# Kernel optimization log

Hardware: AMD Instinct MI355X
Metric: run time of the kernel (lower is better)

The kernel has to match this reference:

```python
import jax, jax.numpy as jnp
import numpy as np

K0 = 5.0
ISIZE = (1024.0, 1024.0)  # image (h, w) from ishape
POOL = (7, 7)


def crop_and_resize(feat, boxes, pool):
    """TF tf.image.crop_and_resize (bilinear, extrapolation_value=0) for a single
    image. feat: [H, W, C]; boxes: [N, 4] normalized [y1, x1, y2, x2].
    Returns [N, ph, pw, C]."""
    H, W, C = feat.shape
    ph, pw = pool
    y1, x1, y2, x2 = boxes[:, 0], boxes[:, 1], boxes[:, 2], boxes[:, 3]
    dt = feat.dtype
    # sample grid (ph>1, pw>1 branch of TF kernel)
    iy = y1[:, None] * (H - 1) + jnp.arange(ph, dtype=dt)[None, :] * ((y2 - y1) * (H - 1) / (ph - 1))[:, None]  # [N, ph]
    ix = x1[:, None] * (W - 1) + jnp.arange(pw, dtype=dt)[None, :] * ((x2 - x1) * (W - 1) / (pw - 1))[:, None]  # [N, pw]
    y0f = jnp.floor(iy)
    x0f = jnp.floor(ix)
    ly = (iy - y0f)[:, :, None, None]
    lx = (ix - x0f)[:, None, :, None]
    y0 = jnp.clip(y0f.astype(jnp.int32), 0, H - 1)
    y1i = jnp.clip(y0f.astype(jnp.int32) + 1, 0, H - 1)
    x0 = jnp.clip(x0f.astype(jnp.int32), 0, W - 1)
    x1i = jnp.clip(x0f.astype(jnp.int32) + 1, 0, W - 1)
    f00 = feat[y0[:, :, None], x0[:, None, :]]   # [N, ph, pw, C]
    f01 = feat[y0[:, :, None], x1i[:, None, :]]
    f10 = feat[y1i[:, :, None], x0[:, None, :]]
    f11 = feat[y1i[:, :, None], x1i[:, None, :]]
    top = f00 + (f01 - f00) * lx
    bot = f10 + (f11 - f10) * lx
    val = top + (bot - top) * ly
    valid = (((iy >= 0) & (iy <= H - 1))[:, :, None, None]
             & ((ix >= 0) & (ix <= W - 1))[:, None, :, None])
    return jnp.where(valid, val, jnp.zeros((), dt))


def setup_inputs() -> dict:
    key = jax.random.key(0)
    kf0, kf1, kf2, kf3, kh, kw, ky, kx = jax.random.split(key, 8)
    C = 256
    feat0 = jax.random.normal(kf0, (1, 256, 256, C), dtype=jnp.float32)
    feat1 = jax.random.normal(kf1, (1, 128, 128, C), dtype=jnp.float32)
    feat2 = jax.random.normal(kf2, (1, 64, 64, C), dtype=jnp.float32)
    feat3 = jax.random.normal(kf3, (1, 32, 32, C), dtype=jnp.float32)
    N = 1000
    # box sizes log-uniform in [16, 512] px so levels 0..3 are all exercised
    h = 2.0 ** jax.random.uniform(kh, (N,), minval=4.0, maxval=9.0)
    w = 2.0 ** jax.random.uniform(kw, (N,), minval=4.0, maxval=9.0)
    y1 = jax.random.uniform(ky, (N,)) * (ISIZE[0] - h)
    x1 = jax.random.uniform(kx, (N,)) * (ISIZE[1] - w)
    rois = jnp.stack([y1, x1, y1 + h, x1 + w], axis=1)[None].astype(jnp.float32)  # [1, N, 4]
    return {"feat0": feat0, "feat1": feat1, "feat2": feat2, "feat3": feat3, "rois": rois}


def reference(feat0, feat1, feat2, feat3, rois):
    r = rois[0]  # [N, 4] = [y1, x1, y2, x2]
    h = r[:, 2] - r[:, 0]
    w = r[:, 3] - r[:, 1]
    lvl = jnp.log(jnp.sqrt(h * w)) / jnp.log(2.0)
    lvl = jnp.clip(jnp.round(lvl - K0).astype(jnp.int32), 0, 3)  # [N]
    scale = jnp.array([ISIZE[0], ISIZE[1], ISIZE[0], ISIZE[1]], dtype=r.dtype)
    norm = jax.lax.stop_gradient(r / scale)  # normbox2d + tf.stop_gradient
    # tf.where/gather_nd per level + concat == stable sort of rois by level
    order = jnp.argsort(lvl, stable=True)
    s_lvl = lvl[order]
    s_box = norm[order]
    feats = [feat0[0], feat1[0], feat2[0], feat3[0]]
    N = r.shape[0]
    out = jnp.zeros((N, POOL[0], POOL[1], feat0.shape[-1]), feat0.dtype)
    for l, f in enumerate(feats):  # fixed 4 FPN levels, structurally distinct shapes
        crops = crop_and_resize(f, s_box, POOL)
        out = jnp.where((s_lvl == l)[:, None, None, None], crops, out)
    return out[None]  # [1, N, ph, pw, C]
```

## Files before the change

### kernel.cpp

```cpp
#include <hip/hip_runtime.h>

#define POOL_H 7
#define POOL_W 7
#define CHANS  256

typedef float v4f __attribute__((ext_vector_type(4)));

__global__ void __launch_bounds__(1024) level_sort_kernel(
    const float* __restrict__ rois, int N,
    int* __restrict__ sorted_lvl, float4* __restrict__ sorted_box)
{
    __shared__ int hist[16][4];

    const int tid  = threadIdx.x;
    const int wave = tid >> 6;
    const int lane = tid & 63;

    int lvl = -1;
    float y1 = 0.f, x1 = 0.f, y2 = 0.f, x2 = 0.f;
    if (tid < N) {
        y1 = rois[tid * 4 + 0];
        x1 = rois[tid * 4 + 1];
        y2 = rois[tid * 4 + 2];
        x2 = rois[tid * 4 + 3];
        float h = y2 - y1;
        float w = x2 - x1;
        float l = logf(sqrtf(h * w)) / logf(2.0f);
        int li = (int)rintf(l - 5.0f);
        lvl = li < 0 ? 0 : (li > 3 ? 3 : li);
    }

    unsigned long long mask[4];
    #pragma unroll
    for (int l = 0; l < 4; ++l) mask[l] = __ballot(lvl == l);
    if (lane == 0) {
        #pragma unroll
        for (int l = 0; l < 4; ++l) hist[wave][l] = __popcll(mask[l]);
    }
    __syncthreads();

    if (lvl >= 0) {
        int pos = __popcll(mask[lvl] & ((1ull << lane) - 1ull));
        for (int w2 = 0; w2 < wave; ++w2) pos += hist[w2][lvl];
        for (int l = 0; l < lvl; ++l)
            #pragma unroll
            for (int w2 = 0; w2 < 16; ++w2) pos += hist[w2][l];

        sorted_lvl[pos] = lvl;
        const float inv = 1.0f / 1024.0f;
        sorted_box[pos] = make_float4(y1 * inv, x1 * inv, y2 * inv, x2 * inv);
    }
}

__global__ void __launch_bounds__(448) roi_align_kernel(
    const float* __restrict__ f0, const float* __restrict__ f1,
    const float* __restrict__ f2, const float* __restrict__ f3,
    const int* __restrict__ sorted_lvl, const float4* __restrict__ sorted_box,
    float* __restrict__ out)
{
    const int n    = blockIdx.x;
    const int py   = threadIdx.x >> 6;
    const int lane = threadIdx.x & 63;

    const int lvl = sorted_lvl[n];
    const float4 box = sorted_box[n];

    const float* feat;
    int HW;
    switch (lvl) {
        case 0:  feat = f0; HW = 256; break;
        case 1:  feat = f1; HW = 128; break;
        case 2:  feat = f2; HW = 64;  break;
        default: feat = f3; HW = 32;  break;
    }
    const float Hm1 = (float)(HW - 1);

    const float sy = (box.z - box.x) * Hm1 * (1.0f / 6.0f);
    const float sx = (box.w - box.y) * Hm1 * (1.0f / 6.0f);

    const float iy  = box.x * Hm1 + (float)py * sy;
    const float y0f = floorf(iy);
    const float ly  = iy - y0f;
    int y0  = (int)y0f;
    int y1i = y0 + 1;
    y0  = min(max(y0,  0), HW - 1);
    y1i = min(max(y1i, 0), HW - 1);
    const bool vy = (iy >= 0.0f) & (iy <= Hm1);

    const float4* row0 = (const float4*)(feat + (size_t)(y0  * HW) * CHANS) + lane;
    const float4* row1 = (const float4*)(feat + (size_t)(y1i * HW) * CHANS) + lane;

    float4* outp = (float4*)(out + (size_t)n * (POOL_H * POOL_W * CHANS))
                   + py * (POOL_W * 64) + lane;

    const float ix_base = box.y * Hm1;

    #pragma unroll
    for (int px = 0; px < POOL_W; ++px) {
        const float ix  = ix_base + (float)px * sx;
        const float x0f = floorf(ix);
        const float lx  = ix - x0f;
        int x0  = (int)x0f;
        int x1i = x0 + 1;
        x0  = min(max(x0,  0), HW - 1);
        x1i = min(max(x1i, 0), HW - 1);
        const bool valid = vy & (ix >= 0.0f) & (ix <= Hm1);

        const float4 f00 = row0[(size_t)x0  * 64];
        const float4 f01 = row0[(size_t)x1i * 64];
        const float4 f10 = row1[(size_t)x0  * 64];
        const float4 f11 = row1[(size_t)x1i * 64];

        float4 val;
        {
            float tx, bx;
            tx = f00.x + (f01.x - f00.x) * lx;
            bx = f10.x + (f11.x - f10.x) * lx;
            val.x = tx + (bx - tx) * ly;
            tx = f00.y + (f01.y - f00.y) * lx;
            bx = f10.y + (f11.y - f10.y) * lx;
            val.y = tx + (bx - tx) * ly;
            tx = f00.z + (f01.z - f00.z) * lx;
            bx = f10.z + (f11.z - f10.z) * lx;
            val.z = tx + (bx - tx) * ly;
            tx = f00.w + (f01.w - f00.w) * lx;
            bx = f10.w + (f11.w - f10.w) * lx;
            val.w = tx + (bx - tx) * ly;
        }
        if (!valid) { val.x = 0.f; val.y = 0.f; val.z = 0.f; val.w = 0.f; }

        v4f vv;
        vv.x = val.x; vv.y = val.y; vv.z = val.z; vv.w = val.w;
        __builtin_nontemporal_store(vv, (v4f*)&outp[px * 64]);
    }
}

extern "C" void kernel_launch(void* const* d_in, const int* in_sizes, int n_in,
                              void* d_out, int out_size, void* d_ws, size_t ws_size,
                              hipStream_t stream) {
    const float* f0   = (const float*)d_in[0];
    const float* f1   = (const float*)d_in[1];
    const float* f2   = (const float*)d_in[2];
    const float* f3   = (const float*)d_in[3];
    const float* rois = (const float*)d_in[4];
    const int N = in_sizes[4] / 4;

    int*    sorted_lvl = (int*)d_ws;
    float4* sorted_box = (float4*)((char*)d_ws + 4096);
    float*  out        = (float*)d_out;

    hipLaunchKernelGGL(level_sort_kernel, dim3(1), dim3(1024), 0, stream,
                       rois, N, sorted_lvl, sorted_box);

    hipLaunchKernelGGL(roi_align_kernel, dim3(N), dim3(448), 0, stream,
                       f0, f1, f2, f3, sorted_lvl, sorted_box, out);
}
```

Measured before the change: 137.9 us.

## Schedule ROI blocks by level and spatial bin with XCD-aware block remapping

The sort kernel now also buckets each ROI by level and a coarse 8x8 spatial bin of its top-left corner, and writes an execution order that groups spatially close ROIs. The align kernel remaps block indices so consecutive blocks in each group of 8 (round-robin across XCDs) take contiguous runs of that order, aiming for better L2 reuse of the feature map per XCD. It also replaces the nontemporal output store with a plain store. This adds a serial prefix scan and shared-memory atomics to the tiny sort kernel, and output writes become scattered by slot.

```diff
diff --git a/kernel.cpp b/kernel.cpp
--- a/kernel.cpp
+++ b/kernel.cpp
@@ -4,19 +4,21 @@
 #define POOL_W 7
 #define CHANS  256
 
-typedef float v4f __attribute__((ext_vector_type(4)));
-
 __global__ void __launch_bounds__(1024) level_sort_kernel(
     const float* __restrict__ rois, int N,
-    int* __restrict__ sorted_lvl, float4* __restrict__ sorted_box)
+    int* __restrict__ sorted_lvl, float4* __restrict__ sorted_box,
+    int* __restrict__ exec_slot)
 {
     __shared__ int hist[16][4];
+    __shared__ int bin[256];
+    __shared__ int binbase[256];
+    __shared__ int bincnt[256];
 
     const int tid  = threadIdx.x;
     const int wave = tid >> 6;
     const int lane = tid & 63;
 
-    int lvl = -1;
+    int lvl = -1, key2 = 0;
     float y1 = 0.f, x1 = 0.f, y2 = 0.f, x2 = 0.f;
     if (tid < N) {
         y1 = rois[tid * 4 + 0];
@@ -28,6 +30,9 @@
         float l = logf(sqrtf(h * w)) / logf(2.0f);
         int li = (int)rintf(l - 5.0f);
         lvl = li < 0 ? 0 : (li > 3 ? 3 : li);
+        int yb = (int)(y1 * (1.0f / 128.0f)); yb = yb < 0 ? 0 : (yb > 7 ? 7 : yb);
+        int xb = (int)(x1 * (1.0f / 128.0f)); xb = xb < 0 ? 0 : (xb > 7 ? 7 : xb);
+        key2 = lvl * 64 + yb * 8 + xb;
     }
 
     unsigned long long mask[4];
@@ -37,10 +42,12 @@
         #pragma unroll
         for (int l = 0; l < 4; ++l) hist[wave][l] = __popcll(mask[l]);
     }
+    if (tid < 256) { bin[tid] = 0; bincnt[tid] = 0; }
     __syncthreads();
 
+    int pos = -1;
     if (lvl >= 0) {
-        int pos = __popcll(mask[lvl] & ((1ull << lane) - 1ull));
+        pos = __popcll(mask[lvl] & ((1ull << lane) - 1ull));
         for (int w2 = 0; w2 < wave; ++w2) pos += hist[w2][lvl];
         for (int l = 0; l < lvl; ++l)
             #pragma unroll
@@ -49,6 +56,19 @@
         sorted_lvl[pos] = lvl;
         const float inv = 1.0f / 1024.0f;
         sorted_box[pos] = make_float4(y1 * inv, x1 * inv, y2 * inv, x2 * inv);
+        atomicAdd(&bin[key2], 1);
+    }
+    __syncthreads();
+
+    if (tid == 0) {
+        int acc = 0;
+        for (int k = 0; k < 256; ++k) { binbase[k] = acc; acc += bin[k]; }
+    }
+    __syncthreads();
+
+    if (lvl >= 0) {
+        int e = binbase[key2] + atomicAdd(&bincnt[key2], 1);
+        exec_slot[e] = pos;
     }
 }
 
@@ -56,14 +76,18 @@
     const float* __restrict__ f0, const float* __restrict__ f1,
     const float* __restrict__ f2, const float* __restrict__ f3,
     const int* __restrict__ sorted_lvl, const float4* __restrict__ sorted_box,
+    const int* __restrict__ exec_slot, int N,
     float* __restrict__ out)
 {
-    const int n    = blockIdx.x;
+    const int b    = blockIdx.x;
     const int py   = threadIdx.x >> 6;
     const int lane = threadIdx.x & 63;
 
-    const int lvl = sorted_lvl[n];
-    const float4 box = sorted_box[n];
+    const int p = (N % 8 == 0) ? ((b & 7) * (N >> 3) + (b >> 3)) : b;
+    const int slot = exec_slot[p];
+
+    const int lvl = sorted_lvl[slot];
+    const float4 box = sorted_box[slot];
 
     const float* feat;
     int HW;
@@ -90,7 +114,7 @@
     const float4* row0 = (const float4*)(feat + (size_t)(y0  * HW) * CHANS) + lane;
     const float4* row1 = (const float4*)(feat + (size_t)(y1i * HW) * CHANS) + lane;
 
-    float4* outp = (float4*)(out + (size_t)n * (POOL_H * POOL_W * CHANS))
+    float4* outp = (float4*)(out + (size_t)slot * (POOL_H * POOL_W * CHANS))
                    + py * (POOL_W * 64) + lane;
 
     const float ix_base = box.y * Hm1;
@@ -129,9 +153,7 @@
         }
         if (!valid) { val.x = 0.f; val.y = 0.f; val.z = 0.f; val.w = 0.f; }
 
-        v4f vv;
-        vv.x = val.x; vv.y = val.y; vv.z = val.z; vv.w = val.w;
-        __builtin_nontemporal_store(vv, (v4f*)&outp[px * 64]);
+        outp[px * 64] = val;
     }
 }
 
@@ -147,11 +169,12 @@
 
     int*    sorted_lvl = (int*)d_ws;
     float4* sorted_box = (float4*)((char*)d_ws + 4096);
+    int*    exec_slot  = (int*)((char*)d_ws + 24576);
     float*  out        = (float*)d_out;
 
     hipLaunchKernelGGL(level_sort_kernel, dim3(1), dim3(1024), 0, stream,
-                       rois, N, sorted_lvl, sorted_box);
+                       rois, N, sorted_lvl, sorted_box, exec_slot);
 
     hipLaunchKernelGGL(roi_align_kernel, dim3(N), dim3(448), 0, stream,
-                       f0, f1, f2, f3, sorted_lvl, sorted_box, out);
+                       f0, f1, f2, f3, sorted_lvl, sorted_box, exec_slot, N, out);
 }
```

Result: slower. 144.9 us (+5.1%).
